# Performance work log

Hardware: AMD Instinct MI355X
Metric: run time of the kernel (lower is better)

Reference implementation:

```python
import jax, jax.numpy as jnp
import numpy as np

B, T, D = 2, 2048, 2048
NH, NKV = 16, 4
HD = D // NH  # 128
BASE, TSL = 10000.0, 1024


def rotary_tables(T, hd, base=BASE, tsl=TSL):
    # Matches Rotary.forward with rd == hd (rd=0 in __init__ -> full head dim).
    ar = jnp.arange(0, hd, 2, dtype=jnp.float32) / hd
    if T <= tsl:
        inv = 1.0 / (base ** ar)
    else:
        # NTK-style rescale; note right-assoc exponent in original torch code:
        # 1/(base * (T/tsl) ** ((rd/(rd-2)) ** ar))
        inv = 1.0 / (base * jnp.power(T / tsl, jnp.power(hd / (hd - 2.0), ar)))
    f = jnp.outer(jnp.arange(T, dtype=jnp.float32), inv)  # [T, hd//2]
    cos = jnp.cos(f)[None, :, None, :]  # [1,T,1,hd//2]
    sin = jnp.sin(f)[None, :, None, :]
    return cos, sin


def apply_rope(x, cos, sin):
    # full-dim rope: split halves, rotate
    h = x.shape[-1] // 2
    x1, x2 = x[..., :h], x[..., h:]
    return jnp.concatenate((x1 * cos + x2 * sin, -x1 * sin + x2 * cos), axis=-1)


def rms_norm(x):
    eps = jnp.finfo(x.dtype).eps
    return x * jax.lax.rsqrt(jnp.mean(x * x, axis=-1, keepdims=True) + eps)


def setup_inputs() -> dict:
    key = jax.random.key(0)
    k0, k1, k2, k3, k4 = jax.random.split(key, 5)
    s = 0.02
    return {
        "x": jax.random.normal(k0, (B, T, D), jnp.float32),
        "qw": jax.random.normal(k1, (NH * HD, D), jnp.float32) * s,
        "kw": jax.random.normal(k2, (NKV * HD, D), jnp.float32) * s,
        "vw": jax.random.normal(k3, (NKV * HD, D), jnp.float32) * s,
        "ow": jax.random.normal(k4, (D, D), jnp.float32) * s,
        "qg": jnp.ones((NH,), jnp.float32),
    }


def reference(x, qw, kw, vw, ow, qg):
    Bx, Tx, Dx = x.shape
    q = (x @ qw.T).reshape(Bx, Tx, NH, HD)
    k = (x @ kw.T).reshape(Bx, Tx, NKV, HD)
    v = (x @ vw.T).reshape(Bx, Tx, NKV, HD)
    q = rms_norm(q)
    k = rms_norm(k)
    cos, sin = rotary_tables(Tx, HD)
    q = apply_rope(q, cos, sin) * qg[None, None, :, None]
    k = apply_rope(k, cos, sin)
    # GQA: repeat kv heads
    r = NH // NKV
    k = jnp.repeat(k, r, axis=2)  # [B,T,NH,HD]
    v = jnp.repeat(v, r, axis=2)
    scale = 1.0 / jnp.sqrt(jnp.asarray(HD, q.dtype))
    scores = jnp.einsum("bqhd,bkhd->bhqk", q, k) * scale  # [B,NH,T,T]
    causal = jnp.tril(jnp.ones((Tx, Tx), dtype=bool))
    scores = jnp.where(causal[None, None, :, :], scores, jnp.asarray(-jnp.inf, scores.dtype))
    attn = jax.nn.softmax(scores, axis=-1)
    y = jnp.einsum("bhqk,bkhd->bqhd", attn, v)  # [B,T,NH,HD]
    return y.reshape(Bx, Tx, Dx) @ ow.T
```

## Files before the change

### kernel.cpp

```cpp
#include <hip/hip_runtime.h>
#include <hip/hip_bf16.h>
#include <stdint.h>


typedef __attribute__((ext_vector_type(8))) short short8;
typedef __attribute__((ext_vector_type(4))) float f32x4;
typedef __attribute__((ext_vector_type(16))) float f32x16;

#define GLOAD16(gp, lp) \
  __builtin_amdgcn_global_load_lds((const __attribute__((address_space(1))) void*)(gp), \
                                   (__attribute__((address_space(3))) void*)(lp), 16, 0, 0)

#define BAR() do { asm volatile("" ::: "memory"); __builtin_amdgcn_s_barrier(); asm volatile("" ::: "memory"); } while (0)

__device__ __forceinline__ float bf2f(unsigned short u) {
  union { unsigned int i; float f; } v; v.i = ((unsigned int)u) << 16; return v.f;
}
__device__ __forceinline__ unsigned short f2bf(float f) {
  union { float fl; unsigned int i; } v; v.fl = f;
  unsigned int r = v.i + 0x7fffu + ((v.i >> 16) & 1u);
  return (unsigned short)(r >> 16);
}
__device__ __forceinline__ unsigned pk2(float a, float b) {
  return (unsigned)f2bf(a) | ((unsigned)f2bf(b) << 16);
}

__global__ __launch_bounds__(256) void prep_kernel(
    const float* __restrict__ x, const float* __restrict__ qw,
    const float* __restrict__ kw, const float* __restrict__ vw,
    const float* __restrict__ ow,
    unsigned short* __restrict__ xb, unsigned short* __restrict__ wqkv,
    unsigned short* __restrict__ owb, float* __restrict__ cost, float* __restrict__ sint) {
  const int NX = 2097152;
  const int NW = 1572864;
  const int NO = 1048576;
  const int NT = 131072;
  int tid = blockIdx.x * 256 + threadIdx.x;
  if (tid < NX) {
    float4 v = ((const float4*)x)[tid];
    uint2 o; o.x = pk2(v.x, v.y); o.y = pk2(v.z, v.w);
    ((uint2*)xb)[tid] = o;
  } else if (tid < NX + NW) {
    int i = tid - NX; int e = i * 4;
    const float* src = (e < 4194304) ? (qw + e)
                     : (e < 5242880) ? (kw + (e - 4194304))
                                     : (vw + (e - 5242880));
    float4 v = *(const float4*)src;
    uint2 o; o.x = pk2(v.x, v.y); o.y = pk2(v.z, v.w);
    ((uint2*)wqkv)[i] = o;
  } else if (tid < NX + NW + NO) {
    int i = tid - NX - NW;
    float4 v = ((const float4*)ow)[i];
    uint2 o; o.x = pk2(v.x, v.y); o.y = pk2(v.z, v.w);
    ((uint2*)owb)[i] = o;
  } else if (tid < NX + NW + NO + NT) {
    int i = tid - NX - NW - NO;
    int t = i >> 6, j = i & 63;
    float e = exp2f(0.02272008f * (float)j * (1.0f / 64.0f));
    float inv = 1.0f / (10000.0f * exp2f(e));
    float f = (float)t * inv;
    cost[i] = cosf(f);
    sint[i] = sinf(f);
  }
}

template <int IM, int NB, int OUTF>
__global__ __launch_bounds__(512) void gemm8ph(const unsigned short* __restrict__ A,
                                               const unsigned short* __restrict__ Bw,
                                               void* __restrict__ Cp,
                                               int MT, int NTn, int N, int K) {
  extern __shared__ char smc[];
  constexpr int S = IM * 8;
  constexpr int IQ = IM / 2;
  constexpr int JQ = NB / 128;
  constexpr int ASZ = IM * 2048;
  constexpr int BSZ = NB * 64;
  constexpr int DB = 2 * ASZ + 2 * BSZ;
  constexpr int AL = (IM * 128) / 512;
  constexpr int BL = NB / 128;
  constexpr int VMCN = AL + 2 * BL;
  const int tid = threadIdx.x;
  const int l = tid & 63, w = tid >> 6;
  const int lane_r = l & 15, lane_g = l >> 4;
  const int wr = w >> 2, wc = w & 3;

  int qch = (MT * NTn) >> 3;
  int orig = blockIdx.x;
  int wgid = (orig & 7) * qch + (orig >> 3);
  int by = wgid / NTn, bx = wgid - by * NTn;
  const int m0 = by * IM * 32, n0 = bx * NB;

  f32x4 acc[IM][2 * JQ];
#pragma unroll
  for (int i = 0; i < IM; ++i)
#pragma unroll
    for (int j = 0; j < 2 * JQ; ++j) acc[i][j] = {0.f, 0.f, 0.f, 0.f};

  const unsigned short* srcA[AL]; int ldA[AL];
#pragma unroll
  for (int t = 0; t < AL; ++t) {
    int idx = t * 512 + tid;
    int rc = idx >> 3, kc = idx & 7;
    int wrp = rc >= S ? 1 : 0, rr = rc & (S - 1);
    int row = wrp * 2 * S + rr;
    srcA[t] = A + (size_t)(m0 + row) * K + (kc ^ (rc & 7)) * 8;
    ldA[t] = idx * 16;
  }
  const unsigned short* srcB[BL]; int ldB[BL];
#pragma unroll
  for (int t = 0; t < BL; ++t) {
    int idx = t * 512 + tid;
    int rc = idx >> 3, kc = idx & 7;
    int g16 = rc >> 4;
    int nrow = (g16 / JQ) * (NB / 4) + (g16 % JQ) * 16 + (rc & 15);
    srcB[t] = Bw + (size_t)(n0 + nrow) * K + (kc ^ (rc & 7)) * 8;
    ldB[t] = idx * 16;
  }
  const int SK = S * K, JK = (NB / 8) * K;

  auto STA = [&](int kt, int ih, int dqb) {
    char* d = smc + dqb + ih * ASZ;
#pragma unroll
    for (int t = 0; t < AL; ++t) GLOAD16(srcA[t] + kt + ih * SK, d + ldA[t]);
  };
  auto STB = [&](int kt, int jh, int dqb) {
    char* d = smc + dqb + 2 * ASZ + jh * BSZ;
#pragma unroll
    for (int t = 0; t < BL; ++t) GLOAD16(srcB[t] + kt + jh * JK, d + ldB[t]);
  };

  int oA[IQ][2], oB[JQ][2];
#pragma unroll
  for (int iq = 0; iq < IQ; ++iq)
#pragma unroll
    for (int ks = 0; ks < 2; ++ks) {
      int rc = wr * S + iq * 16 + lane_r;
      oA[iq][ks] = rc * 128 + ((ks * 64 + lane_g * 16) ^ ((rc & 7) << 4));
    }
#pragma unroll
  for (int jj = 0; jj < JQ; ++jj)
#pragma unroll
    for (int ks = 0; ks < 2; ++ks) {
      int rc = wc * (NB / 8) + jj * 16 + lane_r;
      oB[jj][ks] = rc * 128 + ((ks * 64 + lane_g * 16) ^ ((rc & 7) << 4));
    }

#define VMC() asm volatile("s_waitcnt vmcnt(%0)" :: "i"(VMCN) : "memory")
#define VM0() asm volatile("s_waitcnt vmcnt(0)" ::: "memory")
#define MM(IH, JH, BR) do { \
    __builtin_amdgcn_s_setprio(1); \
    _Pragma("unroll") \
    for (int iq = 0; iq < IQ; ++iq) \
      _Pragma("unroll") \
      for (int jj = 0; jj < JQ; ++jj) \
        _Pragma("unroll") \
        for (int ks = 0; ks < 2; ++ks) \
          acc[(IH) * IQ + iq][(JH) * JQ + jj] = __builtin_amdgcn_mfma_f32_16x16x32_bf16( \
              af[iq][ks], BR[jj][ks], acc[(IH) * IQ + iq][(JH) * JQ + jj], 0, 0, 0); \
    __builtin_amdgcn_s_setprio(0); } while (0)

  const int NS = K >> 6;
  STA(0, 0, 0); STB(0, 0, 0); STB(0, 1, 0); STA(0, 1, 0);
  STA(64, 0, DB); STB(64, 0, DB); STB(64, 1, DB);
  VMC();
  BAR();

#pragma unroll 1
  for (int s = 0; s < NS; ++s) {
    const int dq = (s & 1) * DB, dn = DB - dq;
    const char* Ab = smc + dq;
    const char* Bb = Ab + 2 * ASZ;
    short8 af[IQ][2], b0[JQ][2], b1[JQ][2];
    if (s + 1 < NS) STA((s + 1) << 6, 1, dn);
#pragma unroll
    for (int iq = 0; iq < IQ; ++iq)
#pragma unroll
      for (int ks = 0; ks < 2; ++ks) af[iq][ks] = *(const short8*)(Ab + oA[iq][ks]);
#pragma unroll
    for (int jj = 0; jj < JQ; ++jj)
#pragma unroll
      for (int ks = 0; ks < 2; ++ks) b0[jj][ks] = *(const short8*)(Bb + oB[jj][ks]);
    MM(0, 0, b0);
    BAR();
    if (s + 2 < NS) STA((s + 2) << 6, 0, dq);
#pragma unroll
    for (int jj = 0; jj < JQ; ++jj)
#pragma unroll
      for (int ks = 0; ks < 2; ++ks) b1[jj][ks] = *(const short8*)(Bb + BSZ + oB[jj][ks]);
    MM(0, 1, b1);
    BAR();
    if (s + 2 < NS) STB((s + 2) << 6, 0, dq);
#pragma unroll
    for (int iq = 0; iq < IQ; ++iq)
#pragma unroll
      for (int ks = 0; ks < 2; ++ks) af[iq][ks] = *(const short8*)(Ab + ASZ + oA[iq][ks]);
    MM(1, 0, b0);
    BAR();
    if (s + 2 < NS) STB((s + 2) << 6, 1, dq);
    MM(1, 1, b1);
    if (s + 2 < NS) VMC(); else VM0();
    BAR();
  }
#undef VMC
#undef VM0
#undef MM

#pragma unroll
  for (int ih = 0; ih < 2; ++ih)
#pragma unroll
    for (int iq = 0; iq < IQ; ++iq) {
      int row = m0 + wr * 2 * S + ih * S + iq * 16 + lane_g * 4;
#pragma unroll
      for (int jh = 0; jh < 2; ++jh)
#pragma unroll
        for (int jj = 0; jj < JQ; ++jj) {
          int col = n0 + wc * (NB / 4) + jh * (NB / 8) + jj * 16 + lane_r;
#pragma unroll
          for (int r = 0; r < 4; ++r) {
            float v = acc[ih * IQ + iq][jh * JQ + jj][r];
            if (OUTF)
              ((float*)Cp)[(size_t)(row + r) * N + col] = v;
            else
              ((unsigned short*)Cp)[(size_t)(row + r) * N + col] = f2bf(v);
          }
        }
    }
}

__global__ __launch_bounds__(256) void normrope_vt_kernel(unsigned short* __restrict__ qkv,
                                                          const float* __restrict__ cost,
                                                          const float* __restrict__ sint,
                                                          const float* __restrict__ qg,
                                                          unsigned short* __restrict__ vtg) {
  __shared__ unsigned short tile[64][132];
  int bid = blockIdx.x;
  const int tid = threadIdx.x;
  if (bid < 20480) {
    const int l = tid & 63, w = tid >> 6;
    int row = bid * 4 + w;
    int tok = row / 20, hh = row - tok * 20;
    int t = tok & 2047;
    bool isq = hh < 16;
    int col0 = isq ? hh * 128 : 2048 + (hh - 16) * 128;
    unsigned short* p = qkv + (size_t)tok * 3072 + col0 + 2 * l;
    unsigned int u = *(const unsigned int*)p;
    float x0 = bf2f((unsigned short)(u & 0xffffu));
    float x1 = bf2f((unsigned short)(u >> 16));
    float ss = x0 * x0 + x1 * x1;
#pragma unroll
    for (int m = 1; m < 64; m <<= 1) ss += __shfl_xor(ss, m);
    float rn = rsqrtf(ss * (1.0f / 128.0f) + 1.1920928955078125e-07f);
    float n0 = x0 * rn, n1 = x1 * rn;
    float p0 = __shfl_xor(n0, 32);
    float p1 = __shfl_xor(n1, 32);
    int jj = (2 * l) & 63;
    float c0 = cost[t * 64 + jj], c1 = cost[t * 64 + jj + 1];
    float s0 = sint[t * 64 + jj], s1 = sint[t * 64 + jj + 1];
    float o0, o1;
    if (l < 32) { o0 = n0 * c0 + p0 * s0; o1 = n1 * c1 + p1 * s1; }
    else        { o0 = -p0 * s0 + n0 * c0; o1 = -p1 * s1 + n1 * c1; }
    if (isq) { float g = qg[hh] * 0.08838834764831845f * 1.4426950408889634f; o0 *= g; o1 *= g; }
    *(unsigned int*)p = pk2(o0, o1);
  } else {
    int bid2 = bid - 20480;
    int pan = bid2 & 7, tt = bid2 >> 3;
    int b = pan >> 2, kvh = pan & 3;
    int t0 = tt * 64;
    const unsigned short* src = qkv + ((size_t)(b * 2048 + t0)) * 3072 + 2560 + kvh * 128;
#pragma unroll
    for (int i = 0; i < 8; ++i) {
      int idx = i * 256 + tid;
      int row = idx >> 5, c4 = idx & 31;
      uint2 v = *(const uint2*)(src + (size_t)row * 3072 + c4 * 4);
      *(uint2*)&tile[row][c4 * 4] = v;
    }
    __syncthreads();
    unsigned short* dst = vtg + (size_t)pan * 262144 + t0;
#pragma unroll
    for (int i = 0; i < 8; ++i) {
      int idx = i * 256 + tid;
      int d = idx >> 4, tc = idx & 15;
      unsigned short a0 = tile[tc * 4 + 0][d], a1 = tile[tc * 4 + 1][d];
      unsigned short a2 = tile[tc * 4 + 2][d], a3 = tile[tc * 4 + 3][d];
      uint2 o; o.x = (unsigned)a0 | ((unsigned)a1 << 16);
      o.y = (unsigned)a2 | ((unsigned)a3 << 16);
      *(uint2*)(dst + (size_t)d * 2048 + tc * 4) = o;
    }
  }
}

__global__ __launch_bounds__(256, 2) void attn_fa8(const unsigned short* __restrict__ qkv,
                                                   const unsigned short* __restrict__ vtg,
                                                   unsigned short* __restrict__ y) {
  extern __shared__ char smc[];
  const int tid = threadIdx.x;
  const int l = tid & 63, w = tid >> 6;
  const int lq = l & 31, hi = l >> 5;

  int bid = blockIdx.x;
  int n8 = bid & 255;
  int pan = n8 & 7;
  int b = pan >> 2, kvh = pan & 3;
  int idx2 = n8 >> 3;
  int h = kvh * 4 + (idx2 & 3);
  int pairIdx = idx2 >> 2;
  const int qt = (bid >> 8) ? pairIdx : 15 - pairIdx;
  const size_t rowbase = (size_t)b * 2048;
  const unsigned short* kvK = qkv + rowbase * 3072;
  const unsigned short* vtp = vtg + (size_t)pan * 262144;

  int kg[4], vg[4], sl[4];
#pragma unroll
  for (int t = 0; t < 4; ++t) {
    int idx = t * 256 + tid;
    { int row = idx >> 4, c = idx & 15, gc = c ^ (row & 7);
      kg[t] = row * 3072 + 2048 + kvh * 128 + gc * 8; }
    { int d = idx >> 3, c = idx & 7, gc = c ^ (d & 7);
      vg[t] = d * 2048 + gc * 8; }
    sl[t] = idx * 16;
  }
  const int swq = (lq & 7) << 4;
  int oxd[8];
#pragma unroll
  for (int ds = 0; ds < 8; ++ds) oxd[ds] = (ds * 32 + hi * 16) ^ swq;
  const int krow = lq * 256;
  const int vrow = lq * 128;

  auto STAGE = [&](int tile, int bufsel) {
    const unsigned short* srcK = kvK + (size_t)tile * 64 * 3072;
    const unsigned short* srcV = vtp + tile * 64;
    char* kd = smc + bufsel * 16384;
    char* vd = smc + 32768 + bufsel * 16384;
#pragma unroll
    for (int t = 0; t < 4; ++t) {
      GLOAD16(srcK + kg[t], kd + sl[t]);
      GLOAD16(srcV + vg[t], vd + sl[t]);
    }
  };

  const int q0 = qt * 128;
  const int nkb = 2 * qt + 2;
  const int wrow0 = q0 + w * 32;
  const int qrow = wrow0 + lq;

  STAGE(0, 0);
  short8 qf[8];
#pragma unroll
  for (int ds = 0; ds < 8; ++ds)
    qf[ds] = *(const short8*)(qkv + (rowbase + qrow) * 3072 + h * 128 + ds * 16 + hi * 8);

  f32x16 acc[4];
#pragma unroll
  for (int dt = 0; dt < 4; ++dt)
#pragma unroll
    for (int jj = 0; jj < 16; ++jj) acc[dt][jj] = 0.f;
  float mrun = -1e30f, lrun = 0.f;

  __syncthreads();

#pragma unroll 1
  for (int kb = 0; kb < nkb; ++kb) {
    const int cur = kb & 1;
    if (kb + 1 < nkb) STAGE(kb + 1, cur ^ 1);
    const int j0 = kb * 64;
    if (j0 <= wrow0 + 31) {
      const int kbb = cur * 16384;
      const int vbb = 32768 + cur * 16384;
      f32x16 s0, s1;
#pragma unroll
      for (int jj = 0; jj < 16; ++jj) { s0[jj] = 0.f; s1[jj] = 0.f; }
      __builtin_amdgcn_s_setprio(1);
#pragma unroll
      for (int ds = 0; ds < 8; ++ds) {
        short8 kf = *(const short8*)(smc + kbb + krow + oxd[ds]);
        s0 = __builtin_amdgcn_mfma_f32_32x32x16_bf16(kf, qf[ds], s0, 0, 0, 0);
      }
#pragma unroll
      for (int ds = 0; ds < 8; ++ds) {
        short8 kf = *(const short8*)(smc + kbb + 8192 + krow + oxd[ds]);
        s1 = __builtin_amdgcn_mfma_f32_32x32x16_bf16(kf, qf[ds], s1, 0, 0, 0);
      }
      __builtin_amdgcn_s_setprio(0);
      const int rq = qrow - j0;
      if (j0 + 63 > wrow0) {
#pragma unroll
        for (int jj = 0; jj < 16; ++jj) {
          int kl = (jj & 3) + 8 * (jj >> 2) + 4 * hi;
          s0[jj] = (kl > rq) ? -1e30f : s0[jj];
          s1[jj] = (kl + 32 > rq) ? -1e30f : s1[jj];
        }
      }
      float pmax = s0[0];
#pragma unroll
      for (int jj = 0; jj < 16; ++jj) pmax = fmaxf(pmax, fmaxf(s0[jj], s1[jj]));
      pmax = fmaxf(pmax, __shfl_xor(pmax, 32));
      if (!__all(pmax - mrun <= 11.5f)) {
        float mn = fmaxf(mrun, pmax);
        float corr = exp2f(mrun - mn);
        lrun *= corr;
#pragma unroll
        for (int dt = 0; dt < 4; ++dt)
#pragma unroll
          for (int jj = 0; jj < 16; ++jj) acc[dt][jj] *= corr;
        mrun = mn;
      }
      float rs = 0.f;
#pragma unroll
      for (int jj = 0; jj < 16; ++jj) {
        s0[jj] = exp2f(s0[jj] - mrun); rs += s0[jj];
        s1[jj] = exp2f(s1[jj] - mrun); rs += s1[jj];
      }
      rs += __shfl_xor(rs, 32);
      lrun += rs;
      unsigned r0[8], r1[8];
#pragma unroll
      for (int j = 0; j < 4; ++j) {
        asm("v_cvt_pk_bf16_f32 %0, %1, %2" : "=v"(r0[2 * j]) : "v"(s0[4 * j]), "v"(s0[4 * j + 1]));
        asm("v_cvt_pk_bf16_f32 %0, %1, %2" : "=v"(r0[2 * j + 1]) : "v"(s0[4 * j + 2]), "v"(s0[4 * j + 3]));
        asm("v_cvt_pk_bf16_f32 %0, %1, %2" : "=v"(r1[2 * j]) : "v"(s1[4 * j]), "v"(s1[4 * j + 1]));
        asm("v_cvt_pk_bf16_f32 %0, %1, %2" : "=v"(r1[2 * j + 1]) : "v"(s1[4 * j + 2]), "v"(s1[4 * j + 3]));
      }
      __builtin_amdgcn_s_setprio(1);
#pragma unroll
      for (int ksl = 0; ksl < 4; ++ksl) {
        unsigned* rr = (ksl < 2) ? r0 : r1;
        int kk = ksl & 1;
        unsigned w0 = rr[4 * kk], w2 = rr[4 * kk + 2];
        asm("v_permlane32_swap_b32 %0, %1" : "+v"(w0), "+v"(w2));
        unsigned w1 = rr[4 * kk + 1], w3 = rr[4 * kk + 3];
        asm("v_permlane32_swap_b32 %0, %1" : "+v"(w1), "+v"(w3));
        union { unsigned u[4]; short8 s8; } pu;
        pu.u[0] = w0; pu.u[1] = w1; pu.u[2] = w2; pu.u[3] = w3;
        short8 pf = pu.s8;
#pragma unroll
        for (int dt = 0; dt < 4; ++dt) {
          short8 vf = *(const short8*)(smc + vbb + dt * 4096 + vrow + oxd[ksl]);
          acc[dt] = __builtin_amdgcn_mfma_f32_32x32x16_bf16(vf, pf, acc[dt], 0, 0, 0);
        }
      }
      __builtin_amdgcn_s_setprio(0);
    }
    __syncthreads();
  }
  float linv = 1.0f / lrun;
  unsigned short* yrow = y + (rowbase + qrow) * 2048 + h * 128;
#pragma unroll
  for (int dt = 0; dt < 4; ++dt)
#pragma unroll
    for (int m = 0; m < 4; ++m) {
      uint2 o;
      o.x = pk2(acc[dt][4 * m] * linv, acc[dt][4 * m + 1] * linv);
      o.y = pk2(acc[dt][4 * m + 2] * linv, acc[dt][4 * m + 3] * linv);
      *(uint2*)(yrow + dt * 32 + m * 8 + hi * 4) = o;
    }
}

extern "C" void kernel_launch(void* const* d_in, const int* in_sizes, int n_in,
                              void* d_out, int out_size, void* d_ws, size_t ws_size,
                              hipStream_t stream) {
  (void)in_sizes; (void)n_in; (void)out_size; (void)ws_size;
  const float* x  = (const float*)d_in[0];
  const float* qw = (const float*)d_in[1];
  const float* kw = (const float*)d_in[2];
  const float* vw = (const float*)d_in[3];
  const float* ow = (const float*)d_in[4];
  const float* qg = (const float*)d_in[5];

  char* ws = (char*)d_ws;
  unsigned short* xb   = (unsigned short*)(ws + 0);
  unsigned short* vtg  = (unsigned short*)(ws + 0);
  unsigned short* wqkv = (unsigned short*)(ws + 16777216);
  unsigned short* owb  = (unsigned short*)(ws + 29360128);
  unsigned short* qkvb = (unsigned short*)(ws + 37748736);
  unsigned short* y    = (unsigned short*)(ws + 62914560);
  float* cost          = (float*)(ws + 79691776);
  float* sint          = (float*)(ws + 80216064);

  prep_kernel<<<18944, 256, 0, stream>>>(x, qw, kw, vw, ow, xb, wqkv, owb, cost, sint);
  gemm8ph<4, 384, 0><<<256, 512, 131072, stream>>>(xb, wqkv, qkvb, 32, 8, 3072, 2048);
  normrope_vt_kernel<<<20736, 256, 0, stream>>>(qkvb, cost, sint, qg, vtg);
  attn_fa8<<<512, 256, 65536, stream>>>(qkvb, vtg, y);
  gemm8ph<4, 256, 1><<<256, 512, 98304, stream>>>(y, owb, d_out, 32, 8, 2048, 2048);
}
```

Baseline: 196.1 us.

## Split KV tile across warp halves and process paired q-tiles per block

The attention kernel now launches 256 blocks of 512 threads, and each block handles both q-tiles of a causal-balanced pair in sequence rather than spreading them over separate blocks. Within a block, two groups of four warps each take half of a 128-row KV tile. Their partial softmax states (max, sum, accumulator) are merged through shared memory before the output is written. This is meant to cut the number of KV loop iterations and balance the causal workload per CU, at the cost of a cross-warp merge, more shared memory (128KB), and one block per CU.

```diff
diff --git a/kernel.cpp b/kernel.cpp
--- a/kernel.cpp
+++ b/kernel.cpp
@@ -289,22 +289,21 @@
   }
 }
 
-__global__ __launch_bounds__(256, 2) void attn_fa8(const unsigned short* __restrict__ qkv,
-                                                   const unsigned short* __restrict__ vtg,
-                                                   unsigned short* __restrict__ y) {
+__global__ __launch_bounds__(512) void attn_fa10(const unsigned short* __restrict__ qkv,
+                                                 const unsigned short* __restrict__ vtg,
+                                                 unsigned short* __restrict__ y) {
   extern __shared__ char smc[];
   const int tid = threadIdx.x;
   const int l = tid & 63, w = tid >> 6;
   const int lq = l & 31, hi = l >> 5;
-
-  int bid = blockIdx.x;
-  int n8 = bid & 255;
-  int pan = n8 & 7;
+  const int g = w & 3, hh = w >> 2;
+
+  int n = blockIdx.x;
+  int pan = n & 7;
   int b = pan >> 2, kvh = pan & 3;
-  int idx2 = n8 >> 3;
+  int idx2 = n >> 3;
   int h = kvh * 4 + (idx2 & 3);
   int pairIdx = idx2 >> 2;
-  const int qt = (bid >> 8) ? pairIdx : 15 - pairIdx;
   const size_t rowbase = (size_t)b * 2048;
   const unsigned short* kvK = qkv + rowbase * 3072;
   const unsigned short* vtp = vtg + (size_t)pan * 262144;
@@ -312,25 +311,30 @@
   int kg[4], vg[4], sl[4];
 #pragma unroll
   for (int t = 0; t < 4; ++t) {
-    int idx = t * 256 + tid;
-    { int row = idx >> 4, c = idx & 15, gc = c ^ (row & 7);
-      kg[t] = row * 3072 + 2048 + kvh * 128 + gc * 8; }
-    { int d = idx >> 3, c = idx & 7, gc = c ^ (d & 7);
-      vg[t] = d * 2048 + gc * 8; }
+    int idx = t * 512 + tid;
+    int row = idx >> 4, c = idx & 15, gc = c ^ (row & 7);
+    kg[t] = row * 3072 + 2048 + kvh * 128 + gc * 8;
+    vg[t] = row * 2048 + gc * 8;
     sl[t] = idx * 16;
   }
   const int swq = (lq & 7) << 4;
-  int oxd[8];
-#pragma unroll
-  for (int ds = 0; ds < 8; ++ds) oxd[ds] = (ds * 32 + hi * 16) ^ swq;
-  const int krow = lq * 256;
-  const int vrow = lq * 128;
+  const int krow = (hh * 64 + lq) * 256;
+  int oxk[8];
+#pragma unroll
+  for (int ds = 0; ds < 8; ++ds) oxk[ds] = (ds * 32 + hi * 16) ^ swq;
+  const int vrow = lq * 256;
+  int oxv[4];
+#pragma unroll
+  for (int ksl = 0; ksl < 4; ++ksl) oxv[ksl] = (hh * 128 + ksl * 32 + hi * 16) ^ swq;
+  const int mab = (g * 64 + l) * 256;
+  const int mlb = 65536 + (g * 64 + l) * 8;
+  const int lsw = (l & 7) << 4;
 
   auto STAGE = [&](int tile, int bufsel) {
-    const unsigned short* srcK = kvK + (size_t)tile * 64 * 3072;
-    const unsigned short* srcV = vtp + tile * 64;
-    char* kd = smc + bufsel * 16384;
-    char* vd = smc + 32768 + bufsel * 16384;
+    const unsigned short* srcK = kvK + (size_t)tile * 128 * 3072;
+    const unsigned short* srcV = vtp + tile * 128;
+    char* kd = smc + bufsel * 32768;
+    char* vd = smc + 65536 + bufsel * 32768;
 #pragma unroll
     for (int t = 0; t < 4; ++t) {
       GLOAD16(srcK + kg[t], kd + sl[t]);
@@ -338,121 +342,154 @@
     }
   };
 
-  const int q0 = qt * 128;
-  const int nkb = 2 * qt + 2;
-  const int wrow0 = q0 + w * 32;
-  const int qrow = wrow0 + lq;
-
-  STAGE(0, 0);
-  short8 qf[8];
-#pragma unroll
-  for (int ds = 0; ds < 8; ++ds)
-    qf[ds] = *(const short8*)(qkv + (rowbase + qrow) * 3072 + h * 128 + ds * 16 + hi * 8);
-
-  f32x16 acc[4];
-#pragma unroll
-  for (int dt = 0; dt < 4; ++dt)
-#pragma unroll
-    for (int jj = 0; jj < 16; ++jj) acc[dt][jj] = 0.f;
-  float mrun = -1e30f, lrun = 0.f;
-
-  __syncthreads();
-
 #pragma unroll 1
-  for (int kb = 0; kb < nkb; ++kb) {
-    const int cur = kb & 1;
-    if (kb + 1 < nkb) STAGE(kb + 1, cur ^ 1);
-    const int j0 = kb * 64;
-    if (j0 <= wrow0 + 31) {
-      const int kbb = cur * 16384;
-      const int vbb = 32768 + cur * 16384;
-      f32x16 s0, s1;
-#pragma unroll
-      for (int jj = 0; jj < 16; ++jj) { s0[jj] = 0.f; s1[jj] = 0.f; }
-      __builtin_amdgcn_s_setprio(1);
-#pragma unroll
-      for (int ds = 0; ds < 8; ++ds) {
-        short8 kf = *(const short8*)(smc + kbb + krow + oxd[ds]);
-        s0 = __builtin_amdgcn_mfma_f32_32x32x16_bf16(kf, qf[ds], s0, 0, 0, 0);
+  for (int phase = 0; phase < 2; ++phase) {
+    const int qt = phase ? pairIdx : 15 - pairIdx;
+    const int q0 = qt * 128;
+    const int nkb = qt + 1;
+    const int wrow0 = q0 + g * 32;
+    const int qrow = wrow0 + lq;
+
+    STAGE(0, 0);
+    short8 qf[8];
+#pragma unroll
+    for (int ds = 0; ds < 8; ++ds)
+      qf[ds] = *(const short8*)(qkv + (rowbase + qrow) * 3072 + h * 128 + ds * 16 + hi * 8);
+
+    f32x16 acc[4];
+#pragma unroll
+    for (int dt = 0; dt < 4; ++dt)
+#pragma unroll
+      for (int jj = 0; jj < 16; ++jj) acc[dt][jj] = 0.f;
+    float mrun = -1e30f, lrun = 0.f;
+
+    __syncthreads();
+
+#pragma unroll 1
+    for (int kb = 0; kb < nkb; ++kb) {
+      const int cur = kb & 1;
+      if (kb + 1 < nkb) STAGE(kb + 1, cur ^ 1);
+      const int j0 = kb * 128;
+      if (j0 + hh * 64 <= wrow0) {
+        const int kbb = cur * 32768;
+        const int vbb = 65536 + cur * 32768;
+        f32x16 s0, s1;
+#pragma unroll
+        for (int jj = 0; jj < 16; ++jj) { s0[jj] = 0.f; s1[jj] = 0.f; }
+        __builtin_amdgcn_s_setprio(1);
+#pragma unroll
+        for (int ds = 0; ds < 8; ++ds) {
+          short8 kf = *(const short8*)(smc + kbb + krow + oxk[ds]);
+          s0 = __builtin_amdgcn_mfma_f32_32x32x16_bf16(kf, qf[ds], s0, 0, 0, 0);
+        }
+#pragma unroll
+        for (int ds = 0; ds < 8; ++ds) {
+          short8 kf = *(const short8*)(smc + kbb + 8192 + krow + oxk[ds]);
+          s1 = __builtin_amdgcn_mfma_f32_32x32x16_bf16(kf, qf[ds], s1, 0, 0, 0);
+        }
+        __builtin_amdgcn_s_setprio(0);
+        const int rq = qrow - j0 - hh * 64;
+        if (rq < 63) {
+#pragma unroll
+          for (int jj = 0; jj < 16; ++jj) {
+            int kl = (jj & 3) + 8 * (jj >> 2) + 4 * hi;
+            s0[jj] = (kl > rq) ? -1e30f : s0[jj];
+            s1[jj] = (kl + 32 > rq) ? -1e30f : s1[jj];
+          }
+        }
+        float pmax = s0[0];
+#pragma unroll
+        for (int jj = 0; jj < 16; ++jj) pmax = fmaxf(pmax, fmaxf(s0[jj], s1[jj]));
+        pmax = fmaxf(pmax, __shfl_xor(pmax, 32));
+        if (!__all(pmax - mrun <= 11.5f)) {
+          float mn = fmaxf(mrun, pmax);
+          float corr = exp2f(mrun - mn);
+          lrun *= corr;
+#pragma unroll
+          for (int dt = 0; dt < 4; ++dt)
+#pragma unroll
+            for (int jj = 0; jj < 16; ++jj) acc[dt][jj] *= corr;
+          mrun = mn;
+        }
+        float rs = 0.f;
+#pragma unroll
+        for (int jj = 0; jj < 16; ++jj) {
+          s0[jj] = exp2f(s0[jj] - mrun); rs += s0[jj];
+          s1[jj] = exp2f(s1[jj] - mrun); rs += s1[jj];
+        }
+        rs += __shfl_xor(rs, 32);
+        lrun += rs;
+        unsigned r0[8], r1[8];
+#pragma unroll
+        for (int j = 0; j < 4; ++j) {
+          asm("v_cvt_pk_bf16_f32 %0, %1, %2" : "=v"(r0[2 * j]) : "v"(s0[4 * j]), "v"(s0[4 * j + 1]));
+          asm("v_cvt_pk_bf16_f32 %0, %1, %2" : "=v"(r0[2 * j + 1]) : "v"(s0[4 * j + 2]), "v"(s0[4 * j + 3]));
+          asm("v_cvt_pk_bf16_f32 %0, %1, %2" : "=v"(r1[2 * j]) : "v"(s1[4 * j]), "v"(s1[4 * j + 1]));
+          asm("v_cvt_pk_bf16_f32 %0, %1, %2" : "=v"(r1[2 * j + 1]) : "v"(s1[4 * j + 2]), "v"(s1[4 * j + 3]));
+        }
+        __builtin_amdgcn_s_setprio(1);
+#pragma unroll
+        for (int ksl = 0; ksl < 4; ++ksl) {
+          unsigned* rr = (ksl < 2) ? r0 : r1;
+          int kk = ksl & 1;
+          unsigned w0 = rr[4 * kk], w2 = rr[4 * kk + 2];
+          asm("v_permlane32_swap_b32 %0, %1" : "+v"(w0), "+v"(w2));
+          unsigned w1 = rr[4 * kk + 1], w3 = rr[4 * kk + 3];
+          asm("v_permlane32_swap_b32 %0, %1" : "+v"(w1), "+v"(w3));
+          union { unsigned u[4]; short8 s8; } pu;
+          pu.u[0] = w0; pu.u[1] = w1; pu.u[2] = w2; pu.u[3] = w3;
+          short8 pf = pu.s8;
+#pragma unroll
+          for (int dt = 0; dt < 4; ++dt) {
+            short8 vf = *(const short8*)(smc + vbb + dt * 8192 + vrow + oxv[ksl]);
+            acc[dt] = __builtin_amdgcn_mfma_f32_32x32x16_bf16(vf, pf, acc[dt], 0, 0, 0);
+          }
+        }
+        __builtin_amdgcn_s_setprio(0);
       }
-#pragma unroll
-      for (int ds = 0; ds < 8; ++ds) {
-        short8 kf = *(const short8*)(smc + kbb + 8192 + krow + oxd[ds]);
-        s1 = __builtin_amdgcn_mfma_f32_32x32x16_bf16(kf, qf[ds], s1, 0, 0, 0);
-      }
-      __builtin_amdgcn_s_setprio(0);
-      const int rq = qrow - j0;
-      if (j0 + 63 > wrow0) {
-#pragma unroll
-        for (int jj = 0; jj < 16; ++jj) {
-          int kl = (jj & 3) + 8 * (jj >> 2) + 4 * hi;
-          s0[jj] = (kl > rq) ? -1e30f : s0[jj];
-          s1[jj] = (kl + 32 > rq) ? -1e30f : s1[jj];
-        }
-      }
-      float pmax = s0[0];
-#pragma unroll
-      for (int jj = 0; jj < 16; ++jj) pmax = fmaxf(pmax, fmaxf(s0[jj], s1[jj]));
-      pmax = fmaxf(pmax, __shfl_xor(pmax, 32));
-      if (!__all(pmax - mrun <= 11.5f)) {
-        float mn = fmaxf(mrun, pmax);
-        float corr = exp2f(mrun - mn);
-        lrun *= corr;
-#pragma unroll
-        for (int dt = 0; dt < 4; ++dt)
-#pragma unroll
-          for (int jj = 0; jj < 16; ++jj) acc[dt][jj] *= corr;
-        mrun = mn;
-      }
-      float rs = 0.f;
-#pragma unroll
-      for (int jj = 0; jj < 16; ++jj) {
-        s0[jj] = exp2f(s0[jj] - mrun); rs += s0[jj];
-        s1[jj] = exp2f(s1[jj] - mrun); rs += s1[jj];
-      }
-      rs += __shfl_xor(rs, 32);
-      lrun += rs;
-      unsigned r0[8], r1[8];
-#pragma unroll
-      for (int j = 0; j < 4; ++j) {
-        asm("v_cvt_pk_bf16_f32 %0, %1, %2" : "=v"(r0[2 * j]) : "v"(s0[4 * j]), "v"(s0[4 * j + 1]));
-        asm("v_cvt_pk_bf16_f32 %0, %1, %2" : "=v"(r0[2 * j + 1]) : "v"(s0[4 * j + 2]), "v"(s0[4 * j + 3]));
-        asm("v_cvt_pk_bf16_f32 %0, %1, %2" : "=v"(r1[2 * j]) : "v"(s1[4 * j]), "v"(s1[4 * j + 1]));
-        asm("v_cvt_pk_bf16_f32 %0, %1, %2" : "=v"(r1[2 * j + 1]) : "v"(s1[4 * j + 2]), "v"(s1[4 * j + 3]));
-      }
-      __builtin_amdgcn_s_setprio(1);
-#pragma unroll
-      for (int ksl = 0; ksl < 4; ++ksl) {
-        unsigned* rr = (ksl < 2) ? r0 : r1;
-        int kk = ksl & 1;
-        unsigned w0 = rr[4 * kk], w2 = rr[4 * kk + 2];
-        asm("v_permlane32_swap_b32 %0, %1" : "+v"(w0), "+v"(w2));
-        unsigned w1 = rr[4 * kk + 1], w3 = rr[4 * kk + 3];
-        asm("v_permlane32_swap_b32 %0, %1" : "+v"(w1), "+v"(w3));
-        union { unsigned u[4]; short8 s8; } pu;
-        pu.u[0] = w0; pu.u[1] = w1; pu.u[2] = w2; pu.u[3] = w3;
-        short8 pf = pu.s8;
-#pragma unroll
-        for (int dt = 0; dt < 4; ++dt) {
-          short8 vf = *(const short8*)(smc + vbb + dt * 4096 + vrow + oxd[ksl]);
-          acc[dt] = __builtin_amdgcn_mfma_f32_32x32x16_bf16(vf, pf, acc[dt], 0, 0, 0);
-        }
-      }
-      __builtin_amdgcn_s_setprio(0);
+      __syncthreads();
+    }
+    if (hh) {
+#pragma unroll
+      for (int dt = 0; dt < 4; ++dt)
+#pragma unroll
+        for (int q4 = 0; q4 < 4; ++q4) {
+          f32x4 v = {acc[dt][4 * q4], acc[dt][4 * q4 + 1], acc[dt][4 * q4 + 2], acc[dt][4 * q4 + 3]};
+          *(f32x4*)(smc + mab + ((dt * 64 + q4 * 16) ^ lsw)) = v;
+        }
+      *(float2*)(smc + mlb) = {mrun, lrun};
     }
     __syncthreads();
-  }
-  float linv = 1.0f / lrun;
-  unsigned short* yrow = y + (rowbase + qrow) * 2048 + h * 128;
-#pragma unroll
-  for (int dt = 0; dt < 4; ++dt)
-#pragma unroll
-    for (int m = 0; m < 4; ++m) {
-      uint2 o;
-      o.x = pk2(acc[dt][4 * m] * linv, acc[dt][4 * m + 1] * linv);
-      o.y = pk2(acc[dt][4 * m + 2] * linv, acc[dt][4 * m + 3] * linv);
-      *(uint2*)(yrow + dt * 32 + m * 8 + hi * 4) = o;
-    }
+    if (!hh) {
+      float2 ml = *(const float2*)(smc + mlb);
+      float mx = fmaxf(mrun, ml.x);
+      float sc0 = exp2f(mrun - mx), sc1 = exp2f(ml.x - mx);
+      lrun = lrun * sc0 + ml.y * sc1;
+#pragma unroll
+      for (int dt = 0; dt < 4; ++dt)
+#pragma unroll
+        for (int q4 = 0; q4 < 4; ++q4) {
+          f32x4 v = *(const f32x4*)(smc + mab + ((dt * 64 + q4 * 16) ^ lsw));
+#pragma unroll
+          for (int r = 0; r < 4; ++r)
+            acc[dt][4 * q4 + r] = acc[dt][4 * q4 + r] * sc0 + v[r] * sc1;
+        }
+    }
+    __syncthreads();
+    if (!hh) {
+      float linv = 1.0f / lrun;
+      unsigned short* yrow = y + (rowbase + qrow) * 2048 + h * 128;
+#pragma unroll
+      for (int dt = 0; dt < 4; ++dt)
+#pragma unroll
+        for (int m = 0; m < 4; ++m) {
+          uint2 o;
+          o.x = pk2(acc[dt][4 * m] * linv, acc[dt][4 * m + 1] * linv);
+          o.y = pk2(acc[dt][4 * m + 2] * linv, acc[dt][4 * m + 3] * linv);
+          *(uint2*)(yrow + dt * 32 + m * 8 + hi * 4) = o;
+        }
+    }
+  }
 }
 
 extern "C" void kernel_launch(void* const* d_in, const int* in_sizes, int n_in,
@@ -479,6 +516,6 @@
   prep_kernel<<<18944, 256, 0, stream>>>(x, qw, kw, vw, ow, xb, wqkv, owb, cost, sint);
   gemm8ph<4, 384, 0><<<256, 512, 131072, stream>>>(xb, wqkv, qkvb, 32, 8, 3072, 2048);
   normrope_vt_kernel<<<20736, 256, 0, stream>>>(qkvb, cost, sint, qg, vtg);
-  attn_fa8<<<512, 256, 65536, stream>>>(qkvb, vtg, y);
+  attn_fa10<<<256, 512, 131072, stream>>>(qkvb, vtg, y);
   gemm8ph<4, 256, 1><<<256, 512, 98304, stream>>>(y, owb, d_out, 32, 8, 2048, 2048);
 }
```

New measurement: 186.5 us (median of 3 runs). 1.05x faster.
